# Kernel optimization log

Hardware: AMD Instinct MI355X
Metric: run time of the kernel (lower is better)

Reference implementation:

```python
import jax, jax.numpy as jnp
import numpy as np

DECAY = 0.99
EPS = 1e-05
NUM_EMBEDDINGS = 2048
EMBEDDING_DIM = 512


def setup_inputs() -> dict:
    key = jax.random.key(0)
    k1, k2 = jax.random.split(key)
    z_e = jax.random.normal(k1, (16, 4096, EMBEDDING_DIM), dtype=jnp.float32)
    embedding = jax.random.normal(k2, (NUM_EMBEDDINGS, EMBEDDING_DIM), dtype=jnp.float32)
    cluster_size = jnp.zeros((NUM_EMBEDDINGS,), dtype=jnp.float32)
    embed_avg = embedding  # buffer initialized as a clone of embedding
    return {"z_e": z_e, "embedding": embedding, "cluster_size": cluster_size, "embed_avg": embed_avg}


def reference(z_e, embedding, cluster_size, embed_avg):
    K, D = embedding.shape
    flat = z_e.reshape(-1, D)  # [N, D]
    dist = (jnp.sum(flat * flat, axis=1, keepdims=True)
            - 2.0 * flat @ embedding.T
            + jnp.sum(embedding * embedding, axis=1))
    idx = jnp.argmin(dist, axis=1)  # [N] int
    z_q_raw = embedding[idx].reshape(z_e.shape)

    # EMA cluster statistics (training path). one_hot.T @ flat == segment_sum
    counts = jax.ops.segment_sum(jnp.ones_like(idx, dtype=flat.dtype), idx, num_segments=K)
    embed_sum = jax.ops.segment_sum(flat, idx, num_segments=K)  # [K, D]
    new_cluster_size = DECAY * cluster_size + (1.0 - DECAY) * counts
    new_embed_avg = DECAY * embed_avg + (1.0 - DECAY) * embed_sum
    n = jnp.sum(new_cluster_size)
    cs_smoothed = (new_cluster_size + EPS) / (n + K * EPS) * n
    new_embedding = new_embed_avg / cs_smoothed[:, None]

    # straight-through estimator
    z_q = z_e + jax.lax.stop_gradient(z_q_raw - z_e)
    commit_loss = jnp.mean((jax.lax.stop_gradient(z_e) - z_q) ** 2)
    codebook_loss = jnp.mean((z_e - jax.lax.stop_gradient(z_q)) ** 2)
    vq_loss = codebook_loss + 0.25 * commit_loss
    return (z_q, idx, vq_loss, new_embedding, new_cluster_size, new_embed_avg)
```

## Files before the change

kernel.cpp:

```cpp
#include <hip/hip_runtime.h>

typedef unsigned short ushort_t;
typedef unsigned int u32;
typedef unsigned long long u64;
typedef __attribute__((ext_vector_type(8))) short bf16x8;
typedef __attribute__((ext_vector_type(4))) float f32x4;

#define N_ROWS 65536
#define K_EMB  2048
#define D_DIM  512
#define OFF_ZQ   0
#define OFF_IDX  33554432
#define OFF_LOSS 33619968
#define OFF_EMB  33619969
#define OFF_NCS  34668545
#define OFF_NEA  34670593
#define TAU 1.5f
#define CHUNK 128
#define MAXCHUNK 2560

__device__ __forceinline__ ushort_t f2bf(float f) {
  u32 u = __float_as_uint(f);
  u32 r = (u + 0x7fffu + ((u >> 16) & 1u)) >> 16;
  return (ushort_t)r;
}
__device__ __forceinline__ void glds16(const void* g, void* l) {
  __builtin_amdgcn_global_load_lds((const __attribute__((address_space(1))) u32*)g,
                                   (__attribute__((address_space(3))) u32*)l, 16, 0, 0);
}

#define MERGE4(s1,s2,s3,s4,o1,o2,o3,o4) do {                        \
    u32 x1 = min(s1,o4), x2 = min(s2,o3), x3 = min(s3,o2), x4 = min(s4,o1); \
    u32 t1 = min(x1,x3), t3 = max(x1,x3), t2 = min(x2,x4), t4 = max(x2,x4); \
    s1 = min(t1,t2); s2 = max(t1,t2); s3 = min(t3,t4); s4 = max(t3,t4);     \
  } while (0)

__global__ void prep_kernel(const float* __restrict__ ze, const float* __restrict__ emb,
                            ushort_t* __restrict__ xh, ushort_t* __restrict__ eh,
                            float* __restrict__ enorm, float* __restrict__ counts,
                            float* __restrict__ lossws)
{
  int bx = blockIdx.x;
  int t = threadIdx.x;
  if (bx < 512) {
    int w = t >> 6, l = t & 63;
    int k = bx * 4 + w;
    const float4* row = (const float4*)(emb + (size_t)k * D_DIM);
    float4 a = row[l * 2], b = row[l * 2 + 1];
    ushort4 h0, h1;
    h0.x = f2bf(a.x); h0.y = f2bf(a.y); h0.z = f2bf(a.z); h0.w = f2bf(a.w);
    h1.x = f2bf(b.x); h1.y = f2bf(b.y); h1.z = f2bf(b.z); h1.w = f2bf(b.w);
    ((ushort4*)(eh + (size_t)k * D_DIM))[l * 2] = h0;
    ((ushort4*)(eh + (size_t)k * D_DIM))[l * 2 + 1] = h1;
    float s = a.x*a.x + a.y*a.y + a.z*a.z + a.w*a.w + b.x*b.x + b.y*b.y + b.z*b.z + b.w*b.w;
    #pragma unroll
    for (int off = 32; off >= 1; off >>= 1) s += __shfl_xor(s, off);
    if (l == 0) enorm[k] = s;
  } else {
    int gid = (bx - 512) * 256 + t;
    const float4* zin = (const float4*)ze;
    ushort4* xh4 = (ushort4*)xh;
    for (int g = gid; g < (N_ROWS * D_DIM / 4); g += 8192 * 256) {
      float4 v = zin[g];
      ushort4 h;
      h.x = f2bf(v.x); h.y = f2bf(v.y); h.z = f2bf(v.z); h.w = f2bf(v.w);
      xh4[g] = h;
    }
    if (gid < K_EMB) counts[gid] = 0.0f;
    if (gid == 0) lossws[0] = 0.0f;
  }
}

__global__ __launch_bounds__(256, 2)
void dist_gemm(const ushort_t* __restrict__ xh, const ushort_t* __restrict__ eh,
               const float* __restrict__ enorm, uint4* __restrict__ list)
{
  __shared__ ushort_t Ah[2][128 * 64];
  __shared__ ushort_t Bh[2][128 * 64];
  const int t = threadIdx.x;
  const int w = t >> 6, l = t & 63;
  const int li = l & 15, lg = l >> 4;
  const int row0 = blockIdx.x << 7;
  const int wr = (w >> 1) << 6, wc = (w & 1) << 6;

  u32 offAb[4], offBb[4], ldso[4];
  #pragma unroll
  for (int i = 0; i < 4; ++i) {
    int G = (i << 8) + (w << 6) + l;
    int r = G >> 3, gp = G & 7;
    int cb = gp ^ (r & 7);
    offAb[i] = ((u32)(row0 + r) << 10) + ((u32)cb << 4);
    offBb[i] = ((u32)r << 10) + ((u32)cb << 4);
    ldso[i] = ((u32)((i << 8) + (w << 6))) << 4;
  }
  int aoff[2][4], boff[2][4];
  #pragma unroll
  for (int kblk = 0; kblk < 2; ++kblk) {
    #pragma unroll
    for (int m = 0; m < 4; ++m) {
      int r = wr + (m << 4) + li;
      int c = (kblk << 2) + lg;
      aoff[kblk][m] = (r << 7) + ((c ^ (r & 7)) << 4);
      r = wc + (m << 4) + li;
      boff[kblk][m] = (r << 7) + ((c ^ (r & 7)) << 4);
    }
  }

  u32 cand[16][4];
  #pragma unroll
  for (int mi = 0; mi < 16; ++mi) {
    cand[mi][0] = 0xFFFFFFFFu; cand[mi][1] = 0xFFFFFFFFu;
    cand[mi][2] = 0xFFFFFFFFu; cand[mi][3] = 0xFFFFFFFFu;
  }

  f32x4 acc[4][4];
  #pragma unroll
  for (int m = 0; m < 4; ++m)
    #pragma unroll
    for (int n = 0; n < 4; ++n) acc[m][n] = (f32x4){0.f, 0.f, 0.f, 0.f};

#define STAGE(buf_, s_) do {                                                   \
    u32 sa_ = (u32)(((s_) & 7) << 7);                                          \
    u32 sb_ = (u32)((((s_) >> 3) << 17) + (((s_) & 7) << 7));                  \
    _Pragma("unroll")                                                          \
    for (int i = 0; i < 4; ++i) {                                              \
      glds16((const char*)xh + (offAb[i] + sa_), (char*)Ah[buf_] + ldso[i]);   \
      glds16((const char*)eh + (offBb[i] + sb_), (char*)Bh[buf_] + ldso[i]);   \
    }                                                                          \
  } while (0)

  STAGE(0, 0);
  __syncthreads();
  int buf = 0;
  float en0 = 0.f, en1 = 0.f, en2 = 0.f, en3 = 0.f;

  for (int s = 0; s < 128; ++s) {
    if ((s & 7) == 0) {
      int col0 = (s >> 3) << 7;
      en0 = enorm[col0 + wc + 0  + li];
      en1 = enorm[col0 + wc + 16 + li];
      en2 = enorm[col0 + wc + 32 + li];
      en3 = enorm[col0 + wc + 48 + li];
    }
    if (s != 127) STAGE(buf ^ 1, s + 1);

    #pragma unroll
    for (int kblk = 0; kblk < 2; ++kblk) {
      bf16x8 fah[4], fbh[4];
      #pragma unroll
      for (int m = 0; m < 4; ++m)
        fah[m] = *(const bf16x8*)((const char*)Ah[buf] + aoff[kblk][m]);
      #pragma unroll
      for (int n = 0; n < 4; ++n)
        fbh[n] = *(const bf16x8*)((const char*)Bh[buf] + boff[kblk][n]);
      #pragma unroll
      for (int m = 0; m < 4; ++m)
        #pragma unroll
        for (int n = 0; n < 4; ++n)
          acc[m][n] = __builtin_amdgcn_mfma_f32_16x16x32_bf16(fah[m], fbh[n], acc[m][n], 0, 0, 0);
    }

    if ((s & 7) == 7) {
      int col0 = (s >> 3) << 7;
      const u32 colb = (u32)(col0 + wc + li);
      #pragma unroll
      for (int m = 0; m < 4; ++m)
        #pragma unroll
        for (int i = 0; i < 4; ++i) {
          u32 k0 = (__float_as_uint(fmaf(-2.f, acc[m][0][i], en0)) & 0xFFFFF800u) | colb;
          u32 k1 = (__float_as_uint(fmaf(-2.f, acc[m][1][i], en1)) & 0xFFFFF800u) | (colb + 16u);
          u32 k2 = (__float_as_uint(fmaf(-2.f, acc[m][2][i], en2)) & 0xFFFFF800u) | (colb + 32u);
          u32 k3 = (__float_as_uint(fmaf(-2.f, acc[m][3][i], en3)) & 0xFFFFF800u) | (colb + 48u);
          u32 a = min(k0, k1), b = max(k0, k1);
          u32 c = min(k2, k3), d = max(k2, k3);
          u32 e = min(a, c),  f = max(a, c);
          u32 g = min(b, d),  h = max(b, d);
          u32 q1 = e, q2 = min(f, g), q3 = max(f, g), q4 = h;
          MERGE4(cand[m * 4 + i][0], cand[m * 4 + i][1],
                 cand[m * 4 + i][2], cand[m * 4 + i][3], q1, q2, q3, q4);
          acc[m][0][i] = 0.f; acc[m][1][i] = 0.f;
          acc[m][2][i] = 0.f; acc[m][3][i] = 0.f;
        }
    }
    __syncthreads();
    buf ^= 1;
  }
#undef STAGE

  #pragma unroll
  for (int mi = 0; mi < 16; ++mi) {
    u32 s1 = cand[mi][0], s2 = cand[mi][1], s3 = cand[mi][2], s4 = cand[mi][3];
    #pragma unroll
    for (int off = 1; off <= 8; off <<= 1) {
      u32 o1 = __shfl_xor(s1, off), o2 = __shfl_xor(s2, off);
      u32 o3 = __shfl_xor(s3, off), o4 = __shfl_xor(s4, off);
      MERGE4(s1, s2, s3, s4, o1, o2, o3, o4);
    }
    cand[mi][0] = s1; cand[mi][1] = s2; cand[mi][2] = s3; cand[mi][3] = s4;
  }

  u32* ex = (u32*)Ah;
  if ((w & 1) == 1 && li == 0) {
    #pragma unroll
    for (int m = 0; m < 4; ++m)
      #pragma unroll
      for (int i = 0; i < 4; ++i) {
        int lrow = wr + (m << 4) + (lg << 2) + i;
        uint4 v;
        v.x = cand[m * 4 + i][0]; v.y = cand[m * 4 + i][1];
        v.z = cand[m * 4 + i][2]; v.w = cand[m * 4 + i][3];
        *(uint4*)&ex[lrow << 2] = v;
      }
  }
  __syncthreads();
  if ((w & 1) == 0 && li == 0) {
    #pragma unroll
    for (int m = 0; m < 4; ++m)
      #pragma unroll
      for (int i = 0; i < 4; ++i) {
        int lrow = wr + (m << 4) + (lg << 2) + i;
        const u32* p = &ex[lrow << 2];
        u32 s1 = cand[m * 4 + i][0], s2 = cand[m * 4 + i][1];
        u32 s3 = cand[m * 4 + i][2], s4 = cand[m * 4 + i][3];
        u32 o1 = p[0], o2 = p[1], o3 = p[2], o4 = p[3];
        MERGE4(s1, s2, s3, s4, o1, o2, o3, o4);
        uint4 v; v.x = s1; v.y = s2; v.z = s3; v.w = s4;
        list[row0 + lrow] = v;
      }
  }
}

__global__ void finalize_kernel(const uint4* __restrict__ list, const float* __restrict__ ze,
                                const float* __restrict__ emb, int* __restrict__ wsidx,
                                float* __restrict__ counts, float* __restrict__ o_idx)
{
  int w = threadIdx.x >> 6, l = threadIdx.x & 63;
  int row = blockIdx.x * 4 + w;
  uint4 q = list[row];
  float d1 = __uint_as_float(q.x & 0xFFFFF800u);
  float lim = d1 + TAU;
  bool n2 = (q.y != 0xFFFFFFFFu) && (__uint_as_float(q.y & 0xFFFFF800u) < lim);
  bool n3 = (q.z != 0xFFFFFFFFu) && (__uint_as_float(q.z & 0xFFFFF800u) < lim);
  bool n4 = (q.w != 0xFFFFFFFFu) && (__uint_as_float(q.w & 0xFFFFF800u) < lim);
  int idx;
  if (!(n2 | n3 | n4)) {
    idx = (int)(q.x & 2047u);
  } else {
    double bd = 1e300; int bc = 0x7fffffff;
    const float* xr = ze + (((size_t)row) << 9);
    double xv[8];
    #pragma unroll
    for (int p = 0; p < 8; ++p) xv[p] = (double)xr[(l << 3) + p];
    #pragma unroll
    for (int j = 0; j < 4; ++j) {
      u32 kj = (j == 0) ? q.x : (j == 1) ? q.y : (j == 2) ? q.z : q.w;
      bool ok = (j == 0) || ((kj != 0xFFFFFFFFu) &&
                             (__uint_as_float(kj & 0xFFFFF800u) < lim));
      if (!ok) continue;
      int col = (int)(kj & 2047u);
      const float* er = emb + (((size_t)col) << 9);
      double s = 0.0;
      #pragma unroll
      for (int p = 0; p < 8; ++p) {
        double df = xv[p] - (double)er[(l << 3) + p];
        s += df * df;
      }
      #pragma unroll
      for (int off = 32; off >= 1; off >>= 1) s += __shfl_xor(s, off);
      if (s < bd || (s == bd && col < bc)) { bd = s; bc = col; }
    }
    idx = bc;
  }
  if (l == 0) {
    wsidx[row] = idx;
    o_idx[row] = (float)idx;
    atomicAdd(&counts[idx], 1.0f);
  }
}

__global__ void scan_kernel(const float* __restrict__ counts, const float* __restrict__ cs,
                            u32* __restrict__ offsets, u32* __restrict__ cursor,
                            u32* __restrict__ chunkinfo, u32* __restrict__ ntotal,
                            float* __restrict__ o_ncs, float* __restrict__ inv)
{
  int t = threadIdx.x;
  int c[8]; int s = 0;
  float ncs[8]; float nsum = 0.0f;
  #pragma unroll
  for (int i = 0; i < 8; ++i) {
    int k = t * 8 + i;
    c[i] = (int)counts[k]; s += c[i];
    float v = 0.99f * cs[k] + 0.01f * counts[k];
    ncs[i] = v; o_ncs[k] = v; nsum += v;
  }
  __shared__ int ts[256];
  __shared__ float red[256];
  red[t] = nsum;
  ts[t] = s; __syncthreads();
  for (int off = 1; off < 256; off <<= 1) {
    int v = (t >= off) ? ts[t - off] : 0;
    __syncthreads();
    ts[t] += v;
    __syncthreads();
  }
  for (int h = 128; h >= 1; h >>= 1) { if (t < h) red[t] += red[t + h]; __syncthreads(); }
  float n = red[0];
  float denom = n + 2048.0f * 1e-5f;
  #pragma unroll
  for (int i = 0; i < 8; ++i) {
    float sm = (ncs[i] + 1e-5f) / denom * n;
    inv[t * 8 + i] = 1.0f / sm;
  }
  int run = ts[t] - s;
  int nch[8]; int ns = 0;
  #pragma unroll
  for (int i = 0; i < 8; ++i) {
    offsets[t * 8 + i] = (u32)run;
    cursor[t * 8 + i] = 0;
    run += c[i];
    nch[i] = (c[i] + CHUNK - 1) / CHUNK;
    ns += nch[i];
  }
  __shared__ int ts2[256];
  ts2[t] = ns; __syncthreads();
  for (int off = 1; off < 256; off <<= 1) {
    int v = (t >= off) ? ts2[t - off] : 0;
    __syncthreads();
    ts2[t] += v;
    __syncthreads();
  }
  int cb = ts2[t] - ns;
  #pragma unroll
  for (int i = 0; i < 8; ++i)
    for (int cc = 0; cc < nch[i]; ++cc)
      chunkinfo[cb++] = (u32)(t * 8 + i) | ((u32)cc << 11);
  if (t == 255) *ntotal = (u32)ts2[255];
}

__global__ void scatter_zero_kernel(const int* __restrict__ wsidx, const u32* __restrict__ offsets,
                                    u32* __restrict__ cursor, u32* __restrict__ sorted,
                                    const float* __restrict__ counts, float* __restrict__ esum)
{
  int bx = blockIdx.x;
  int t = threadIdx.x;
  if (bx < 256) {
    int row = bx * 256 + t;
    int idx = wsidx[row];
    u32 pos = atomicAdd(&cursor[idx], 1u);
    sorted[offsets[idx] + pos] = (u32)row;
  } else {
    int k = bx - 256;
    float c = counts[k];
    if (c == 0.0f || c > (float)CHUNK) {
      esum[((size_t)k << 9) + t] = 0.0f;
      esum[((size_t)k << 9) + 256 + t] = 0.0f;
    }
  }
}

__global__ __launch_bounds__(256)
void zq_seg_kernel(const float* __restrict__ ze, const float* __restrict__ emb,
                   const float* __restrict__ ea, const float* __restrict__ inv,
                   const u32* __restrict__ offsets, const float* __restrict__ counts,
                   const u32* __restrict__ sorted, const u32* __restrict__ chunkinfo,
                   const u32* __restrict__ ntotal, float* __restrict__ o_zq,
                   float* __restrict__ esum, float* __restrict__ o_nea,
                   float* __restrict__ lossws)
{
  int cid = blockIdx.x;
  if (cid >= (int)*ntotal) return;
  u32 rec = chunkinfo[cid];
  int k = rec & 2047, c = (int)(rec >> 11);
  int ctotal = (int)counts[k];
  int base = (int)offsets[k] + c * CHUNK;
  int cnt = min(ctotal - c * CHUNK, CHUNK);
  bool multi = ctotal > CHUNK;
  int t = threadIdx.x, w = t >> 6, l = t & 63;
  __shared__ u32 srow[CHUNK];
  __shared__ float sacc[4 * 512];
  __shared__ float sloss[4];
  if (t < cnt) srow[t] = sorted[base + t];
  __syncthreads();
  const float4* e4 = (const float4*)(emb + ((size_t)k << 9));
  float4 ev0 = e4[l * 2], ev1 = e4[l * 2 + 1];
  float a0x=0,a0y=0,a0z=0,a0w=0,a1x=0,a1y=0,a1z=0,a1w=0;
  float lacc = 0.f;
  for (int r = w; r < cnt; r += 4) {
    int row = (int)srow[r];
    const float4* z4 = (const float4*)(ze + ((size_t)row << 9));
    float4 zv0 = z4[l * 2], zv1 = z4[l * 2 + 1];
    float4 q0, q1;
    q0.x = zv0.x + (ev0.x - zv0.x);
    q0.y = zv0.y + (ev0.y - zv0.y);
    q0.z = zv0.z + (ev0.z - zv0.z);
    q0.w = zv0.w + (ev0.w - zv0.w);
    q1.x = zv1.x + (ev1.x - zv1.x);
    q1.y = zv1.y + (ev1.y - zv1.y);
    q1.z = zv1.z + (ev1.z - zv1.z);
    q1.w = zv1.w + (ev1.w - zv1.w);
    float4* zq4 = (float4*)(o_zq + ((size_t)row << 9));
    zq4[l * 2] = q0; zq4[l * 2 + 1] = q1;
    float dx = zv0.x - q0.x, dy = zv0.y - q0.y, dz = zv0.z - q0.z, dw = zv0.w - q0.w;
    lacc += dx*dx + dy*dy + dz*dz + dw*dw;
    dx = zv1.x - q1.x; dy = zv1.y - q1.y; dz = zv1.z - q1.z; dw = zv1.w - q1.w;
    lacc += dx*dx + dy*dy + dz*dz + dw*dw;
    a0x += zv0.x; a0y += zv0.y; a0z += zv0.z; a0w += zv0.w;
    a1x += zv1.x; a1y += zv1.y; a1z += zv1.z; a1w += zv1.w;
  }
  #pragma unroll
  for (int off = 32; off >= 1; off >>= 1) lacc += __shfl_xor(lacc, off);
  if (l == 0) sloss[w] = lacc;
  float* sa = sacc + w * 512 + l * 8;
  sa[0]=a0x; sa[1]=a0y; sa[2]=a0z; sa[3]=a0w; sa[4]=a1x; sa[5]=a1y; sa[6]=a1z; sa[7]=a1w;
  __syncthreads();
  float ikv = inv[k];
  #pragma unroll
  for (int j = 0; j < 2; ++j) {
    int col = t * 2 + j;
    float v = sacc[col] + sacc[512 + col] + sacc[1024 + col] + sacc[1536 + col];
    if (multi) {
      atomicAdd(&esum[((size_t)k << 9) + col], v);
    } else {
      float nea = 0.99f * ea[((size_t)k << 9) + col] + 0.01f * v;
      o_nea[((size_t)k << 9) + col] = nea;
      esum[((size_t)k << 9) + col] = nea * ikv;
    }
  }
  if (t == 0) atomicAdd(lossws, sloss[0] + sloss[1] + sloss[2] + sloss[3]);
}

__global__ void tail_kernel(const float* __restrict__ counts, const float* __restrict__ ea,
                            const float* __restrict__ inv, float* __restrict__ o_emb,
                            float* __restrict__ o_nea, const float* __restrict__ lossws,
                            float* __restrict__ o_loss)
{
  int k = blockIdx.x;
  int t = threadIdx.x;
  if (k == 0 && t == 0) o_loss[0] = lossws[0] * 1.25f / 33554432.0f;
  float c = counts[k];
  bool empty = (c == 0.0f), multi = (c > (float)CHUNK);
  if (!(empty | multi)) return;
  float ikv = inv[k];
  #pragma unroll
  for (int j = 0; j < 2; ++j) {
    int col = t + (j << 8);
    size_t p = ((size_t)k << 9) + col;
    float es = empty ? 0.0f : o_emb[p];
    float nea = 0.99f * ea[p] + 0.01f * es;
    o_nea[p] = nea;
    o_emb[p] = nea * ikv;
  }
}

extern "C" void kernel_launch(void* const* d_in, const int* in_sizes, int n_in,
                              void* d_out, int out_size, void* d_ws, size_t ws_size,
                              hipStream_t stream)
{
  const float* ze  = (const float*)d_in[0];
  const float* emb = (const float*)d_in[1];
  const float* cs  = (const float*)d_in[2];
  const float* ea  = (const float*)d_in[3];
  float* out = (float*)d_out;
  float* o_zq   = out + OFF_ZQ;
  float* o_idx  = out + OFF_IDX;
  float* o_loss = out + OFF_LOSS;
  float* o_emb  = out + OFF_EMB;
  float* o_ncs  = out + OFF_NCS;
  float* o_nea  = out + OFF_NEA;
  ushort_t* xh = (ushort_t*)d_out;
  char* ws = (char*)d_ws;
  ushort_t* ehp = (ushort_t*)ws;
  int* wsidx    = (int*)(ws + 2097152);
  float* counts = (float*)(ws + 2097152 + 262144);
  float* enorm  = counts + 2048;
  float* inv    = enorm + 2048;
  float* lossws = inv + 2048;
  u32* offsets  = (u32*)(lossws + 64);
  u32* cursor   = offsets + 2048;
  u32* sorted   = cursor + 2048;
  u32* chunkinfo= sorted + 65536;
  u32* ntotal   = chunkinfo + MAXCHUNK;
  uint4* list   = (uint4*)(ws + 3145728);

  prep_kernel<<<8704, 256, 0, stream>>>(ze, emb, xh, ehp, enorm, counts, lossws);
  dist_gemm<<<512, 256, 0, stream>>>(xh, ehp, enorm, list);
  finalize_kernel<<<16384, 256, 0, stream>>>(list, ze, emb, wsidx, counts, o_idx);
  scan_kernel<<<1, 256, 0, stream>>>(counts, cs, offsets, cursor, chunkinfo, ntotal,
                                     o_ncs, inv);
  scatter_zero_kernel<<<2304, 256, 0, stream>>>(wsidx, offsets, cursor, sorted,
                                                counts, o_emb);
  zq_seg_kernel<<<MAXCHUNK, 256, 0, stream>>>(ze, emb, ea, inv, offsets, counts, sorted,
                                              chunkinfo, ntotal, o_zq, o_emb, o_nea, lossws);
  tail_kernel<<<2048, 256, 0, stream>>>(counts, ea, inv, o_emb, o_nea, lossws, o_loss);
}
```

Before: 334.4 us.

## Split distance GEMM over column tiles and merge per-tile top-4 in finalize

The distance GEMM used to launch 512 blocks, each sweeping all 2048 codebook columns for one 128-row tile. It now launches 8192 blocks, one per (row tile, column tile) pair, with a swizzled tile order meant to help L2 reuse. Each block writes a top-4 candidate list per column tile into scratch space in the output buffer. The finalize kernel reads those 64 entries per row, takes a wave-wide minimum and ballot, and rechecks near-ties in double precision. The aim is to fill the GPU better, since 512 blocks is few for this chip. In exchange it writes and reads a much larger candidate list (64 entries per row) and reloads A tiles 16 times.

Result: slower. 422.7 us (+26.4%).

```diff
diff --git a/kernel.cpp b/kernel.cpp
--- a/kernel.cpp
+++ b/kernel.cpp
@@ -80,17 +80,22 @@
   const int t = threadIdx.x;
   const int w = t >> 6, l = t & 63;
   const int li = l & 15, lg = l >> 4;
-  const int row0 = blockIdx.x << 7;
+  const int bid = blockIdx.x;
+  const int jj = bid & 63;
+  const int grp = bid >> 6;
+  const int rt = ((grp >> 1) << 3) + (jj & 7);
+  const int ct = ((grp & 1) << 3) + (jj >> 3);
+  const int row0 = rt << 7, col0 = ct << 7;
   const int wr = (w >> 1) << 6, wc = (w & 1) << 6;
 
-  u32 offAb[4], offBb[4], ldso[4];
+  u32 offA[4], offB[4], ldso[4];
   #pragma unroll
   for (int i = 0; i < 4; ++i) {
     int G = (i << 8) + (w << 6) + l;
     int r = G >> 3, gp = G & 7;
     int cb = gp ^ (r & 7);
-    offAb[i] = ((u32)(row0 + r) << 10) + ((u32)cb << 4);
-    offBb[i] = ((u32)r << 10) + ((u32)cb << 4);
+    offA[i] = ((u32)(row0 + r) << 10) + ((u32)cb << 4);
+    offB[i] = ((u32)(col0 + r) << 10) + ((u32)cb << 4);
     ldso[i] = ((u32)((i << 8) + (w << 6))) << 4;
   }
   int aoff[2][4], boff[2][4];
@@ -106,12 +111,10 @@
     }
   }
 
-  u32 cand[16][4];
-  #pragma unroll
-  for (int mi = 0; mi < 16; ++mi) {
-    cand[mi][0] = 0xFFFFFFFFu; cand[mi][1] = 0xFFFFFFFFu;
-    cand[mi][2] = 0xFFFFFFFFu; cand[mi][3] = 0xFFFFFFFFu;
-  }
+  const float en0 = enorm[col0 + wc + 0  + li];
+  const float en1 = enorm[col0 + wc + 16 + li];
+  const float en2 = enorm[col0 + wc + 32 + li];
+  const float en3 = enorm[col0 + wc + 48 + li];
 
   f32x4 acc[4][4];
   #pragma unroll
@@ -120,30 +123,21 @@
     for (int n = 0; n < 4; ++n) acc[m][n] = (f32x4){0.f, 0.f, 0.f, 0.f};
 
 #define STAGE(buf_, s_) do {                                                   \
-    u32 sa_ = (u32)(((s_) & 7) << 7);                                          \
-    u32 sb_ = (u32)((((s_) >> 3) << 17) + (((s_) & 7) << 7));                  \
+    u32 sa_ = (u32)((s_) << 7);                                                \
     _Pragma("unroll")                                                          \
     for (int i = 0; i < 4; ++i) {                                              \
-      glds16((const char*)xh + (offAb[i] + sa_), (char*)Ah[buf_] + ldso[i]);   \
-      glds16((const char*)eh + (offBb[i] + sb_), (char*)Bh[buf_] + ldso[i]);   \
+      glds16((const char*)xh + (offA[i] + sa_), (char*)Ah[buf_] + ldso[i]);    \
+      glds16((const char*)eh + (offB[i] + sa_), (char*)Bh[buf_] + ldso[i]);    \
     }                                                                          \
   } while (0)
 
   STAGE(0, 0);
   __syncthreads();
   int buf = 0;
-  float en0 = 0.f, en1 = 0.f, en2 = 0.f, en3 = 0.f;
-
-  for (int s = 0; s < 128; ++s) {
-    if ((s & 7) == 0) {
-      int col0 = (s >> 3) << 7;
-      en0 = enorm[col0 + wc + 0  + li];
-      en1 = enorm[col0 + wc + 16 + li];
-      en2 = enorm[col0 + wc + 32 + li];
-      en3 = enorm[col0 + wc + 48 + li];
-    }
-    if (s != 127) STAGE(buf ^ 1, s + 1);
-
+
+  #pragma unroll
+  for (int s = 0; s < 8; ++s) {
+    if (s != 7) STAGE(buf ^ 1, s + 1);
     #pragma unroll
     for (int kblk = 0; kblk < 2; ++kblk) {
       bf16x8 fah[4], fbh[4];
@@ -159,45 +153,35 @@
         for (int n = 0; n < 4; ++n)
           acc[m][n] = __builtin_amdgcn_mfma_f32_16x16x32_bf16(fah[m], fbh[n], acc[m][n], 0, 0, 0);
     }
-
-    if ((s & 7) == 7) {
-      int col0 = (s >> 3) << 7;
-      const u32 colb = (u32)(col0 + wc + li);
-      #pragma unroll
-      for (int m = 0; m < 4; ++m)
-        #pragma unroll
-        for (int i = 0; i < 4; ++i) {
-          u32 k0 = (__float_as_uint(fmaf(-2.f, acc[m][0][i], en0)) & 0xFFFFF800u) | colb;
-          u32 k1 = (__float_as_uint(fmaf(-2.f, acc[m][1][i], en1)) & 0xFFFFF800u) | (colb + 16u);
-          u32 k2 = (__float_as_uint(fmaf(-2.f, acc[m][2][i], en2)) & 0xFFFFF800u) | (colb + 32u);
-          u32 k3 = (__float_as_uint(fmaf(-2.f, acc[m][3][i], en3)) & 0xFFFFF800u) | (colb + 48u);
-          u32 a = min(k0, k1), b = max(k0, k1);
-          u32 c = min(k2, k3), d = max(k2, k3);
-          u32 e = min(a, c),  f = max(a, c);
-          u32 g = min(b, d),  h = max(b, d);
-          u32 q1 = e, q2 = min(f, g), q3 = max(f, g), q4 = h;
-          MERGE4(cand[m * 4 + i][0], cand[m * 4 + i][1],
-                 cand[m * 4 + i][2], cand[m * 4 + i][3], q1, q2, q3, q4);
-          acc[m][0][i] = 0.f; acc[m][1][i] = 0.f;
-          acc[m][2][i] = 0.f; acc[m][3][i] = 0.f;
-        }
-    }
     __syncthreads();
     buf ^= 1;
   }
 #undef STAGE
 
-  #pragma unroll
-  for (int mi = 0; mi < 16; ++mi) {
-    u32 s1 = cand[mi][0], s2 = cand[mi][1], s3 = cand[mi][2], s4 = cand[mi][3];
-    #pragma unroll
-    for (int off = 1; off <= 8; off <<= 1) {
-      u32 o1 = __shfl_xor(s1, off), o2 = __shfl_xor(s2, off);
-      u32 o3 = __shfl_xor(s3, off), o4 = __shfl_xor(s4, off);
-      MERGE4(s1, s2, s3, s4, o1, o2, o3, o4);
-    }
-    cand[mi][0] = s1; cand[mi][1] = s2; cand[mi][2] = s3; cand[mi][3] = s4;
-  }
+  const u32 colb = (u32)(col0 + wc + li);
+  u32 myq[16][4];
+  #pragma unroll
+  for (int m = 0; m < 4; ++m)
+    #pragma unroll
+    for (int i = 0; i < 4; ++i) {
+      u32 k0 = (__float_as_uint(fmaf(-2.f, acc[m][0][i], en0)) & 0xFFFFF800u) | colb;
+      u32 k1 = (__float_as_uint(fmaf(-2.f, acc[m][1][i], en1)) & 0xFFFFF800u) | (colb + 16u);
+      u32 k2 = (__float_as_uint(fmaf(-2.f, acc[m][2][i], en2)) & 0xFFFFF800u) | (colb + 32u);
+      u32 k3 = (__float_as_uint(fmaf(-2.f, acc[m][3][i], en3)) & 0xFFFFF800u) | (colb + 48u);
+      u32 a = min(k0, k1), b = max(k0, k1);
+      u32 c = min(k2, k3), d = max(k2, k3);
+      u32 e = min(a, c),  f = max(a, c);
+      u32 g = min(b, d),  h = max(b, d);
+      u32 s1 = e, s2 = min(f, g), s3 = max(f, g), s4 = h;
+      #pragma unroll
+      for (int off = 1; off <= 8; off <<= 1) {
+        u32 o1 = __shfl_xor(s1, off), o2 = __shfl_xor(s2, off);
+        u32 o3 = __shfl_xor(s3, off), o4 = __shfl_xor(s4, off);
+        MERGE4(s1, s2, s3, s4, o1, o2, o3, o4);
+      }
+      myq[m * 4 + i][0] = s1; myq[m * 4 + i][1] = s2;
+      myq[m * 4 + i][2] = s3; myq[m * 4 + i][3] = s4;
+    }
 
   u32* ex = (u32*)Ah;
   if ((w & 1) == 1 && li == 0) {
@@ -207,8 +191,8 @@
       for (int i = 0; i < 4; ++i) {
         int lrow = wr + (m << 4) + (lg << 2) + i;
         uint4 v;
-        v.x = cand[m * 4 + i][0]; v.y = cand[m * 4 + i][1];
-        v.z = cand[m * 4 + i][2]; v.w = cand[m * 4 + i][3];
+        v.x = myq[m * 4 + i][0]; v.y = myq[m * 4 + i][1];
+        v.z = myq[m * 4 + i][2]; v.w = myq[m * 4 + i][3];
         *(uint4*)&ex[lrow << 2] = v;
       }
   }
@@ -220,44 +204,44 @@
       for (int i = 0; i < 4; ++i) {
         int lrow = wr + (m << 4) + (lg << 2) + i;
         const u32* p = &ex[lrow << 2];
-        u32 s1 = cand[m * 4 + i][0], s2 = cand[m * 4 + i][1];
-        u32 s3 = cand[m * 4 + i][2], s4 = cand[m * 4 + i][3];
+        u32 s1 = myq[m * 4 + i][0], s2 = myq[m * 4 + i][1];
+        u32 s3 = myq[m * 4 + i][2], s4 = myq[m * 4 + i][3];
         u32 o1 = p[0], o2 = p[1], o3 = p[2], o4 = p[3];
         MERGE4(s1, s2, s3, s4, o1, o2, o3, o4);
         uint4 v; v.x = s1; v.y = s2; v.z = s3; v.w = s4;
-        list[row0 + lrow] = v;
+        list[(((size_t)(row0 + lrow)) << 4) + ct] = v;
       }
   }
 }
 
-__global__ void finalize_kernel(const uint4* __restrict__ list, const float* __restrict__ ze,
+__global__ void finalize_kernel(const u32* __restrict__ list, const float* __restrict__ ze,
                                 const float* __restrict__ emb, int* __restrict__ wsidx,
                                 float* __restrict__ counts, float* __restrict__ o_idx)
 {
   int w = threadIdx.x >> 6, l = threadIdx.x & 63;
   int row = blockIdx.x * 4 + w;
-  uint4 q = list[row];
-  float d1 = __uint_as_float(q.x & 0xFFFFF800u);
-  float lim = d1 + TAU;
-  bool n2 = (q.y != 0xFFFFFFFFu) && (__uint_as_float(q.y & 0xFFFFF800u) < lim);
-  bool n3 = (q.z != 0xFFFFFFFFu) && (__uint_as_float(q.z & 0xFFFFF800u) < lim);
-  bool n4 = (q.w != 0xFFFFFFFFu) && (__uint_as_float(q.w & 0xFFFFF800u) < lim);
+  u32 ent = list[(((size_t)row) << 6) + l];
+  u32 e1 = ent;
+  #pragma unroll
+  for (int off = 32; off >= 1; off >>= 1) e1 = min(e1, __shfl_xor(e1, off));
+  float d1 = __uint_as_float(e1 & 0xFFFFF800u);
+  float dl = __uint_as_float(ent & 0xFFFFF800u);
+  u64 mask = __ballot(dl < d1 + TAU);
   int idx;
-  if (!(n2 | n3 | n4)) {
-    idx = (int)(q.x & 2047u);
+  if (__popcll(mask) <= 1) {
+    idx = (int)(e1 & 2047u);
   } else {
     double bd = 1e300; int bc = 0x7fffffff;
     const float* xr = ze + (((size_t)row) << 9);
     double xv[8];
     #pragma unroll
     for (int p = 0; p < 8; ++p) xv[p] = (double)xr[(l << 3) + p];
-    #pragma unroll
-    for (int j = 0; j < 4; ++j) {
-      u32 kj = (j == 0) ? q.x : (j == 1) ? q.y : (j == 2) ? q.z : q.w;
-      bool ok = (j == 0) || ((kj != 0xFFFFFFFFu) &&
-                             (__uint_as_float(kj & 0xFFFFF800u) < lim));
-      if (!ok) continue;
-      int col = (int)(kj & 2047u);
+    u64 mm = mask;
+    while (mm) {
+      int j = (int)(__ffsll((long long)mm) - 1);
+      mm &= mm - 1;
+      u32 cj = __shfl(ent, j);
+      int col = (int)(cj & 2047u);
       const float* er = emb + (((size_t)col) << 9);
       double s = 0.0;
       #pragma unroll
@@ -468,6 +452,7 @@
   float* o_ncs  = out + OFF_NCS;
   float* o_nea  = out + OFF_NEA;
   ushort_t* xh = (ushort_t*)d_out;
+  uint4* list  = (uint4*)(out + 16777216);
   char* ws = (char*)d_ws;
   ushort_t* ehp = (ushort_t*)ws;
   int* wsidx    = (int*)(ws + 2097152);
@@ -480,11 +465,10 @@
   u32* sorted   = cursor + 2048;
   u32* chunkinfo= sorted + 65536;
   u32* ntotal   = chunkinfo + MAXCHUNK;
-  uint4* list   = (uint4*)(ws + 3145728);
 
   prep_kernel<<<8704, 256, 0, stream>>>(ze, emb, xh, ehp, enorm, counts, lossws);
-  dist_gemm<<<512, 256, 0, stream>>>(xh, ehp, enorm, list);
-  finalize_kernel<<<16384, 256, 0, stream>>>(list, ze, emb, wsidx, counts, o_idx);
+  dist_gemm<<<8192, 256, 0, stream>>>(xh, ehp, enorm, list);
+  finalize_kernel<<<16384, 256, 0, stream>>>((const u32*)list, ze, emb, wsidx, counts, o_idx);
   scan_kernel<<<1, 256, 0, stream>>>(counts, cs, offsets, cursor, chunkinfo, ntotal,
                                      o_ncs, inv);
   scatter_zero_kernel<<<2304, 256, 0, stream>>>(wsidx, offsets, cursor, sorted,
```
